# Performance work log

Hardware: AMD Instinct MI355X
Metric: run time of the kernel (lower is better)

Reference implementation:

```python
import jax, jax.numpy as jnp
import numpy as np

KINEMATIC_CHAIN = [[0, 2, 5, 8, 11], [0, 1, 4, 7, 10], [0, 3, 6, 9, 12, 15],
                   [9, 14, 17, 19, 21], [9, 13, 16, 18, 20]]
PATHS = [c[1:] for c in KINEMATIC_CHAIN]  # nb_joints == 22 branch


def _gauss_integral(s1, e1, s2, e2):
    # s1,e1,s2,e2: (..., 3) broadcastable; returns (...,) GLI per segment pair
    r13 = s2 - s1
    r14 = e2 - s1
    r23 = s2 - e1
    r24 = e2 - e1
    r12 = e1 - s1
    r34 = e2 - s2
    faces = jnp.stack([jnp.cross(r13, r14), jnp.cross(r14, r24),
                       jnp.cross(r24, r23), jnp.cross(r23, r13)], axis=-2)  # (...,4,3)
    norms = jnp.linalg.norm(faces, axis=-1, keepdims=True)
    nf = jnp.where(norms > 0, faces / jnp.maximum(norms, 1e-30), 0.0)
    dots = jnp.sum(nf * jnp.roll(nf, -1, axis=-2), axis=-1)  # (...,4)
    dots = jnp.clip(dots, -1.0 + 1e-7, 1.0 - 1e-7)
    gli = jnp.sum(jnp.arcsin(dots), axis=-1)
    sign = jnp.sum(jnp.cross(r34, r12) * r13, axis=-1)
    gli = gli * jnp.where(sign <= 0, -1.0, 1.0)
    return gli / (4.0 * jnp.pi)


def _gli_motion(motion1, motion2):
    # motion: (B, F, J, 3) -> (B, F, P*P) summed GLI per path pair
    pair_sums = []
    for p1 in PATHS:
        p1 = np.asarray(p1)
        s1 = motion1[:, :, p1[:-1], None, :]   # (B,F,n1,1,3)
        e1 = motion1[:, :, p1[1:], None, :]
        for p2 in PATHS:
            p2 = np.asarray(p2)
            s2 = motion2[:, :, None, p2[:-1], :]  # (B,F,1,n2,3)
            e2 = motion2[:, :, None, p2[1:], :]
            g = _gauss_integral(s1, e1, s2, e2)   # (B,F,n1,n2)
            pair_sums.append(jnp.sum(g, axis=(-1, -2)))
    return jnp.stack(pair_sums, axis=-1)  # (B, F, 25)


def setup_inputs() -> dict:
    key = jax.random.key(0)
    k1, k2 = jax.random.split(key)
    B, F, J = 32, 1024, 22
    return {
        "motion1": jax.random.normal(k1, (B, F, J, 3), dtype=jnp.float32),
        "motion2": jax.random.normal(k2, (B, F, J, 3), dtype=jnp.float32),
    }


def reference(motion1, motion2):
    gli = _gli_motion(motion1, motion2)            # (B, F, 25)
    vel = jnp.abs(gli[:, 1:] - gli[:, :-1])        # (B, F-1, 25)
    return jnp.max(vel, axis=-1)                   # (B, F-1)
```

## Files before the change

kernel.cpp:

```cpp
#include <hip/hip_runtime.h>
#include <hip/hip_bf16.h>


#define NF 1024
#define NB 32
#define FPB 16
#define JSTRIDE 18

typedef float v2f __attribute__((ext_vector_type(2)));

struct W3 { v2f x, y, z; };

__device__ __forceinline__ v2f FMA2(v2f a, v2f b, v2f c) {
    return __builtin_elementwise_fma(a, b, c);
}
__device__ __forceinline__ W3 wsub(W3 a, W3 b) { return {a.x-b.x, a.y-b.y, a.z-b.z}; }
__device__ __forceinline__ W3 wcross(W3 a, W3 b) {
    return { FMA2(a.y, b.z, -(a.z*b.y)),
             FMA2(a.z, b.x, -(a.x*b.z)),
             FMA2(a.x, b.y, -(a.y*b.x)) };
}
__device__ __forceinline__ v2f wdot(W3 a, W3 b) {
    return FMA2(a.x, b.x, FMA2(a.y, b.y, a.z*b.z));
}
__device__ __forceinline__ v2f rsq_guard(v2f q) {
    v2f r;
    r.x = (q.x > 0.0f) ? __builtin_amdgcn_rsqf(q.x) : 0.0f;
    r.y = (q.y > 0.0f) ? __builtin_amdgcn_rsqf(q.y) : 0.0f;
    return r;
}
__device__ __forceinline__ v2f clamp2(v2f v) {
    const float lo = -1.0f + 1e-7f, hi = 1.0f - 1e-7f;
    v.x = fminf(fmaxf(v.x, lo), hi);
    v.y = fminf(fmaxf(v.y, lo), hi);
    return v;
}
__device__ __forceinline__ v2f asin2(v2f x) {
    v2f ax; ax.x = fabsf(x.x); ax.y = fabsf(x.y);
    v2f p = FMA2(ax, (v2f)(-0.0012624911f), (v2f)(0.0066700901f));
    p = FMA2(ax, p, (v2f)(-0.0170881256f));
    p = FMA2(ax, p, (v2f)( 0.0308918810f));
    p = FMA2(ax, p, (v2f)(-0.0501743046f));
    p = FMA2(ax, p, (v2f)( 0.0889789874f));
    p = FMA2(ax, p, (v2f)(-0.2145988016f));
    p = FMA2(ax, p, (v2f)( 1.5707963050f));
    v2f om = (v2f)(1.0f) - ax;
    v2f s; s.x = __builtin_amdgcn_sqrtf(om.x); s.y = __builtin_amdgcn_sqrtf(om.y);
    v2f r = FMA2(-s, p, (v2f)(1.57079632679f));
    r.x = copysignf(r.x, x.x);
    r.y = copysignf(r.y, x.y);
    return r;
}

__global__ __launch_bounds__(256)
void gli_kernel(const float* __restrict__ m1, const float* __restrict__ m2,
                float* __restrict__ gli)
{
    __shared__ float smem[2 * FPB * 16 * 5];
    float* jT1 = smem;
    float* jT2 = smem + 66 * JSTRIDE;

    const int f0 = blockIdx.x * FPB;
    const int b  = blockIdx.y;
    const int t  = threadIdx.x;

    const size_t mbase = ((size_t)b * NF + f0) * 66;
    for (int i = t; i < FPB * 66; i += 256) {
        int f   = i / 66;
        int off = i - f * 66;
        jT1[off * JSTRIDE + f] = m1[mbase + i];
        jT2[off * JSTRIDE + f] = m2[mbase + i];
    }
    __syncthreads();

    constexpr int seg_a[16] = {2,5,8,  1,4,7,  3,6,9,12,  14,17,19,  13,16,18};
    constexpr int seg_b[16] = {5,8,11, 4,7,10, 6,9,12,15, 17,19,21,  16,18,20};
    constexpr int seg_p[16] = {0,0,0,  1,1,1,  2,2,2,2,   3,3,3,     4,4,4};

    const int half = t >> 7;
    const int kp   = (t >> 4) & 7;
    const int i1   = t & 15;
    const int fc   = 2 * kp;

    const int a1 = seg_a[i1] * 3, b1 = seg_b[i1] * 3;

    #define LD2(base, off) (*(const v2f*)&(base)[(off) * JSTRIDE + fc])
    W3 S1{LD2(jT1, a1), LD2(jT1, a1+1), LD2(jT1, a1+2)};
    W3 E1{LD2(jT1, b1), LD2(jT1, b1+1), LD2(jT1, b1+2)};
    W3 r12 = wsub(E1, S1);

    v2f acc[5] = {(v2f)(0.0f), (v2f)(0.0f), (v2f)(0.0f), (v2f)(0.0f), (v2f)(0.0f)};

    auto body = [&](int i2) {
        const int a2 = seg_a[i2] * 3, b2 = seg_b[i2] * 3;
        W3 S2{LD2(jT2, a2), LD2(jT2, a2+1), LD2(jT2, a2+2)};
        W3 E2{LD2(jT2, b2), LD2(jT2, b2+1), LD2(jT2, b2+2)};

        W3 r13 = wsub(S2, S1);
        W3 r14 = wsub(E2, S1);
        W3 r23 = wsub(S2, E1);
        W3 r24 = wsub(E2, E1);
        W3 r34 = wsub(E2, S2);

        W3 c0 = wcross(r13, r14);
        W3 c1 = wcross(r14, r24);
        W3 c2 = wcross(r24, r23);
        W3 c3 = wcross(r23, r13);

        v2f n0 = wdot(c0, c0), n1 = wdot(c1, c1);
        v2f n2 = wdot(c2, c2), n3 = wdot(c3, c3);

        v2f i01 = rsq_guard(n0 * n1);
        v2f i12 = rsq_guard(n1 * n2);
        v2f i23 = rsq_guard(n2 * n3);
        v2f i30 = rsq_guard(n3 * n0);

        v2f d0 = clamp2(wdot(c0, c1) * i01);
        v2f d1 = clamp2(wdot(c1, c2) * i12);
        v2f d2 = clamp2(wdot(c2, c3) * i23);
        v2f d3 = clamp2(wdot(c3, c0) * i30);

        v2f g = asin2(d0) + asin2(d1) + asin2(d2) + asin2(d3);

        v2f sgn = wdot(wcross(r34, r12), r13);
        g.x = (sgn.x <= 0.0f) ? -g.x : g.x;
        g.y = (sgn.y <= 0.0f) ? -g.y : g.y;

        acc[seg_p[i2]] += g;
    };

    if (half == 0) {
#pragma unroll
        for (int i2 = 0; i2 < 8; ++i2) body(i2);
    } else {
#pragma unroll
        for (int i2 = 8; i2 < 16; ++i2) body(i2);
    }
    #undef LD2

    __syncthreads();

    float* red = smem;
#pragma unroll
    for (int p = 0; p < 5; ++p) {
        red[(((half * FPB) + fc    ) * 16 + i1) * 5 + p] = acc[p].x * 0.07957747154594767f;
        red[(((half * FPB) + fc + 1) * 16 + i1) * 5 + p] = acc[p].y * 0.07957747154594767f;
    }
    __syncthreads();

    constexpr int grp_s[5] = {0, 3, 6, 10, 13};
    constexpr int grp_e[5] = {3, 6, 10, 13, 16};
    for (int item = t; item < FPB * 25; item += 256) {
        int f   = item / 25;
        int bin = item - f * 25;
        int p1 = bin / 5, p2 = bin - p1 * 5;
        float s = 0.0f;
        for (int i = grp_s[p1]; i < grp_e[p1]; ++i)
            s += red[((f          ) * 16 + i) * 5 + p2]
               + red[((f + FPB    ) * 16 + i) * 5 + p2];
        gli[((size_t)b * NF + f0 + f) * 25 + bin] = s;
    }
}

__global__ __launch_bounds__(256)
void vel_kernel(const float* __restrict__ gli, float* __restrict__ out)
{
    const int f = blockIdx.x * blockDim.x + threadIdx.x;
    const int b = blockIdx.y;
    if (f >= NF - 1) return;

    const float* p0 = gli + ((size_t)b * NF + f) * 25;
    float m = 0.0f;
#pragma unroll
    for (int p = 0; p < 25; ++p)
        m = fmaxf(m, fabsf(p0[p + 25] - p0[p]));
    out[(size_t)b * (NF - 1) + f] = m;
}

extern "C" void kernel_launch(void* const* d_in, const int* in_sizes, int n_in,
                              void* d_out, int out_size, void* d_ws, size_t ws_size,
                              hipStream_t stream)
{
    const float* m1 = (const float*)d_in[0];
    const float* m2 = (const float*)d_in[1];
    float* out = (float*)d_out;
    float* gli = (float*)d_ws;

    hipLaunchKernelGGL(gli_kernel, dim3(NF / FPB, NB), dim3(256), 0, stream,
                       m1, m2, gli);
    hipLaunchKernelGGL(vel_kernel, dim3((NF - 1 + 255) / 256, NB), dim3(256),
                       0, stream, gli, out);
}
```

Before: 91.70 us.

## Fuse GLI and velocity kernels using overlapping frame tiles with a halo

Merges the two kernels into one. Each block computes 16 frames but emits 15 outputs, so the frame-to-frame difference can be taken from shared memory. This removes the GLI round trip through global memory and the second launch. In exchange about 1/15 of the GLI work is recomputed, and the grid grows to 69 blocks per batch. It also swaps the guarded rsqrt for a max-floor rsqrt, uses packed min/max for the clamp, and pads the reduction stride to 81 to reduce shared-memory bank conflicts.

```diff
diff --git a/kernel.cpp b/kernel.cpp
--- a/kernel.cpp
+++ b/kernel.cpp
@@ -4,8 +4,10 @@
 
 #define NF 1024
 #define NB 32
-#define FPB 16
+#define FOUT 15
+#define FCMP 16
 #define JSTRIDE 18
+#define RSTRIDE 81
 
 typedef float v2f __attribute__((ext_vector_type(2)));
 
@@ -23,16 +25,16 @@
 __device__ __forceinline__ v2f wdot(W3 a, W3 b) {
     return FMA2(a.x, b.x, FMA2(a.y, b.y, a.z*b.z));
 }
-__device__ __forceinline__ v2f rsq_guard(v2f q) {
+__device__ __forceinline__ v2f rsq_floor(v2f q) {
+    q = __builtin_elementwise_max(q, (v2f)(1.17549435e-38f));
     v2f r;
-    r.x = (q.x > 0.0f) ? __builtin_amdgcn_rsqf(q.x) : 0.0f;
-    r.y = (q.y > 0.0f) ? __builtin_amdgcn_rsqf(q.y) : 0.0f;
+    r.x = __builtin_amdgcn_rsqf(q.x);
+    r.y = __builtin_amdgcn_rsqf(q.y);
     return r;
 }
 __device__ __forceinline__ v2f clamp2(v2f v) {
-    const float lo = -1.0f + 1e-7f, hi = 1.0f - 1e-7f;
-    v.x = fminf(fmaxf(v.x, lo), hi);
-    v.y = fminf(fmaxf(v.y, lo), hi);
+    v = __builtin_elementwise_max(v, (v2f)(-1.0f + 1e-7f));
+    v = __builtin_elementwise_min(v, (v2f)( 1.0f - 1e-7f));
     return v;
 }
 __device__ __forceinline__ v2f asin2(v2f x) {
@@ -52,24 +54,28 @@
     return r;
 }
 
+#define SMEM_FLOATS (2 * FCMP * RSTRIDE + FCMP * 25)
+
 __global__ __launch_bounds__(256)
-void gli_kernel(const float* __restrict__ m1, const float* __restrict__ m2,
-                float* __restrict__ gli)
+void fused_kernel(const float* __restrict__ m1, const float* __restrict__ m2,
+                  float* __restrict__ out)
 {
-    __shared__ float smem[2 * FPB * 16 * 5];
+    __shared__ float smem[SMEM_FLOATS];
     float* jT1 = smem;
     float* jT2 = smem + 66 * JSTRIDE;
 
-    const int f0 = blockIdx.x * FPB;
+    const int f0 = blockIdx.x * FOUT;
     const int b  = blockIdx.y;
     const int t  = threadIdx.x;
 
-    const size_t mbase = ((size_t)b * NF + f0) * 66;
-    for (int i = t; i < FPB * 66; i += 256) {
+    const size_t mbase = (size_t)b * NF * 66;
+    for (int i = t; i < FCMP * 66; i += 256) {
         int f   = i / 66;
         int off = i - f * 66;
-        jT1[off * JSTRIDE + f] = m1[mbase + i];
-        jT2[off * JSTRIDE + f] = m2[mbase + i];
+        int fidx = f0 + f; if (fidx > NF - 1) fidx = NF - 1;
+        size_t ga = mbase + (size_t)fidx * 66 + off;
+        jT1[off * JSTRIDE + f] = m1[ga];
+        jT2[off * JSTRIDE + f] = m2[ga];
     }
     __syncthreads();
 
@@ -110,10 +116,10 @@
         v2f n0 = wdot(c0, c0), n1 = wdot(c1, c1);
         v2f n2 = wdot(c2, c2), n3 = wdot(c3, c3);
 
-        v2f i01 = rsq_guard(n0 * n1);
-        v2f i12 = rsq_guard(n1 * n2);
-        v2f i23 = rsq_guard(n2 * n3);
-        v2f i30 = rsq_guard(n3 * n0);
+        v2f i01 = rsq_floor(n0 * n1);
+        v2f i12 = rsq_floor(n1 * n2);
+        v2f i23 = rsq_floor(n2 * n3);
+        v2f i30 = rsq_floor(n3 * n0);
 
         v2f d0 = clamp2(wdot(c0, c1) * i01);
         v2f d1 = clamp2(wdot(c1, c2) * i12);
@@ -140,41 +146,40 @@
 
     __syncthreads();
 
-    float* red = smem;
+    float* red  = smem;
+    float* gliL = smem + 2 * FCMP * RSTRIDE;
 #pragma unroll
     for (int p = 0; p < 5; ++p) {
-        red[(((half * FPB) + fc    ) * 16 + i1) * 5 + p] = acc[p].x * 0.07957747154594767f;
-        red[(((half * FPB) + fc + 1) * 16 + i1) * 5 + p] = acc[p].y * 0.07957747154594767f;
+        red[(half * FCMP + fc    ) * RSTRIDE + i1 * 5 + p] = acc[p].x * 0.07957747154594767f;
+        red[(half * FCMP + fc + 1) * RSTRIDE + i1 * 5 + p] = acc[p].y * 0.07957747154594767f;
     }
     __syncthreads();
 
     constexpr int grp_s[5] = {0, 3, 6, 10, 13};
     constexpr int grp_e[5] = {3, 6, 10, 13, 16};
-    for (int item = t; item < FPB * 25; item += 256) {
+    for (int item = t; item < FCMP * 25; item += 256) {
         int f   = item / 25;
         int bin = item - f * 25;
         int p1 = bin / 5, p2 = bin - p1 * 5;
         float s = 0.0f;
         for (int i = grp_s[p1]; i < grp_e[p1]; ++i)
-            s += red[((f          ) * 16 + i) * 5 + p2]
-               + red[((f + FPB    ) * 16 + i) * 5 + p2];
-        gli[((size_t)b * NF + f0 + f) * 25 + bin] = s;
+            s += red[(f       ) * RSTRIDE + i * 5 + p2]
+               + red[(f + FCMP) * RSTRIDE + i * 5 + p2];
+        gliL[f * 25 + bin] = s;
     }
-}
+    __syncthreads();
 
-__global__ __launch_bounds__(256)
-void vel_kernel(const float* __restrict__ gli, float* __restrict__ out)
-{
-    const int f = blockIdx.x * blockDim.x + threadIdx.x;
-    const int b = blockIdx.y;
-    if (f >= NF - 1) return;
-
-    const float* p0 = gli + ((size_t)b * NF + f) * 25;
-    float m = 0.0f;
+    if (t < FOUT) {
+        int f = f0 + t;
+        if (f < NF - 1) {
+            const float* s0 = gliL + t * 25;
+            float m = 0.0f;
 #pragma unroll
-    for (int p = 0; p < 25; ++p)
-        m = fmaxf(m, fabsf(p0[p + 25] - p0[p]));
-    out[(size_t)b * (NF - 1) + f] = m;
+            for (int p = 0; p < 25; ++p)
+                m = fmaxf(m, fabsf(s0[p + 25] - s0[p]));
+            out[(size_t)b * (NF - 1) + f] = m;
+        }
+    }
 }
 
 extern "C" void kernel_launch(void* const* d_in, const int* in_sizes, int n_in,
@@ -184,10 +189,8 @@
     const float* m1 = (const float*)d_in[0];
     const float* m2 = (const float*)d_in[1];
     float* out = (float*)d_out;
-    float* gli = (float*)d_ws;
 
-    hipLaunchKernelGGL(gli_kernel, dim3(NF / FPB, NB), dim3(256), 0, stream,
-                       m1, m2, gli);
-    hipLaunchKernelGGL(vel_kernel, dim3((NF - 1 + 255) / 256, NB), dim3(256),
-                       0, stream, gli, out);
+    const int gx = (NF - 1 + FOUT - 1) / FOUT;
+    hipLaunchKernelGGL(fused_kernel, dim3(gx, NB), dim3(256), 0, stream,
+                       m1, m2, out);
 }
```

New measurement: 93.47 us. About the same (+1.9%).
